# Kernel tuning notes

Measured on AMD Instinct MI355X. Metric: run time of the kernel, lower is better.

## Reference

```python
import jax, jax.numpy as jnp
import numpy as np

HEADS = 8
DH = 64          # value head dim == kernel head dim (expansion ratio 1.0)
DIM = 256
BOT = 256        # bottleneck_dim
DOUT = 256
HID = 4 * 256    # MLP hidden (expansion_ratio=4)
EPS_LN = 1e-5
EPS_GN = 1e-6


def layer_norm(x, g, b):
    m = x.mean(axis=-1, keepdims=True)
    v = x.var(axis=-1, keepdims=True)
    return (x - m) / jnp.sqrt(v + EPS_LN) * g + b


def rotate_half(x):
    x1, x2 = jnp.split(x, 2, axis=-1)
    return jnp.concatenate([-x2, x1], axis=-1)


def apply_rope(t, cos, sin):
    return t * cos + rotate_half(t) * sin


def mlp(x, W1, b1, W2, b2):
    return jax.nn.gelu(x @ W1 + b1) @ W2 + b2


def pooling_reducer(x, Win, W1, b1, W2, b2):
    # x: (b, n, m, c); mean-pool over axis 2, then MLP
    x = x @ Win
    x = x.mean(axis=2)
    return mlp(x, W1, b1, W2, b2)


def dp_kernel(x, Wqk, cos, sin):
    # x: (b, n, BOT) -> softmax attention kernel (b, h, n, n)
    b, n, _ = x.shape
    qk = (x @ Wqk).reshape(b, n, 2, HEADS, DH).transpose(0, 3, 2, 1, 4)  # b h 2 n d
    qk = apply_rope(qk, cos, sin)
    q, k = qk[:, :, 0], qk[:, :, 1]
    attn = jnp.einsum('bhid,bhjd->bhij', q, k) * (1.0 / DH)  # softmax scale = 1/dim_head
    return jax.nn.softmax(attn, axis=-1)


def group_norm(x):
    # channels-last GroupNorm(heads groups, affine=False), per position
    b, i, l, _ = x.shape
    xg = x.reshape(b, i, l, HEADS, DH)
    m = xg.mean(axis=-1, keepdims=True)
    v = xg.var(axis=-1, keepdims=True)
    return ((xg - m) / jnp.sqrt(v + EPS_GN)).reshape(b, i, l, HEADS * DH)


def setup_inputs() -> dict:
    key = jax.random.key(0)
    ks = jax.random.split(key, 32)
    B, NY, NX = 4, 128, 128
    s = 0.02
    d = {
        'u': jax.random.normal(ks[0], (B, NY, NX, DIM), jnp.float32),
        'rotary_cos_y': jax.random.uniform(ks[1], (NY, DH), jnp.float32),
        'rotary_sin_y': jax.random.uniform(ks[2], (NY, DH), jnp.float32),
        'rotary_cos_x': jax.random.uniform(ks[3], (NX, DH), jnp.float32),
        'rotary_sin_x': jax.random.uniform(ks[4], (NX, DH), jnp.float32),
        'scalar_cond': jax.random.normal(ks[5], (B,), jnp.float32),
        # norms
        'ln1_g': jnp.ones((DIM,), jnp.float32), 'ln1_b': jnp.zeros((DIM,), jnp.float32),
        'ln2_g': jnp.ones((DIM,), jnp.float32), 'ln2_b': jnp.zeros((DIM,), jnp.float32),
        # to_v
        'Wv': jax.random.normal(ks[6], (DIM, HEADS * DH), jnp.float32) * s,
        # to_y PoolingReducer
        'Wy_in': jax.random.normal(ks[7], (DIM, DIM), jnp.float32) * s,
        'Wy1': jax.random.normal(ks[8], (DIM, HID), jnp.float32) * s,
        'by1': jnp.zeros((HID,), jnp.float32),
        'Wy2': jax.random.normal(ks[9], (HID, BOT), jnp.float32) * s,
        'by2': jnp.zeros((BOT,), jnp.float32),
        # to_x PoolingReducer
        'Wx_in': jax.random.normal(ks[10], (DIM, DIM), jnp.float32) * s,
        'Wx1': jax.random.normal(ks[11], (DIM, HID), jnp.float32) * s,
        'bx1': jnp.zeros((HID,), jnp.float32),
        'Wx2': jax.random.normal(ks[12], (HID, BOT), jnp.float32) * s,
        'bx2': jnp.zeros((BOT,), jnp.float32),
        # kernels
        'Wqk_x': jax.random.normal(ks[13], (BOT, 2 * HEADS * DH), jnp.float32) * s,
        'Wqk_y': jax.random.normal(ks[14], (BOT, 2 * HEADS * DH), jnp.float32) * s,
        # merge head
        'Wm': jax.random.normal(ks[15], (HEADS * DH, DOUT), jnp.float32) * s,
        'bm': jnp.zeros((DOUT,), jnp.float32),
        # ffn
        'Wf1': jax.random.normal(ks[16], (DOUT, 4 * DOUT), jnp.float32) * s,
        'bf1': jnp.zeros((4 * DOUT,), jnp.float32),
        'Wf2': jax.random.normal(ks[17], (4 * DOUT, DOUT), jnp.float32) * s,
        'bf2': jnp.zeros((DOUT,), jnp.float32),
    }
    return d


def reference(u, rotary_cos_y, rotary_sin_y, rotary_cos_x, rotary_sin_x, scalar_cond,
              ln1_g, ln1_b, ln2_g, ln2_b, Wv,
              Wy_in, Wy1, by1, Wy2, by2,
              Wx_in, Wx1, bx1, Wx2, bx2,
              Wqk_x, Wqk_y, Wm, bm, Wf1, bf1, Wf2, bf2):
    b, ny, nx, _ = u.shape
    u_skip = u
    un = layer_norm(u, ln1_g, ln1_b)
    # to_x: transpose grid then pool over (now) second spatial axis -> (b, nx, BOT)
    u_x = pooling_reducer(un.transpose(0, 2, 1, 3), Wx_in, Wx1, bx1, Wx2, bx2)
    # to_y: pool over nx -> (b, ny, BOT)
    u_y = pooling_reducer(un, Wy_in, Wy1, by1, Wy2, by2)
    k_x = dp_kernel(u_x, Wqk_x, rotary_cos_x, rotary_sin_x)  # (b,h,nx,nx)
    k_y = dp_kernel(u_y, Wqk_y, rotary_cos_y, rotary_sin_y)  # (b,h,ny,ny)
    # values: b i l (h c) -> b h i l c
    v = (un @ Wv).reshape(b, ny, nx, HEADS, DH).transpose(0, 3, 1, 2, 4)
    u_phi = jnp.einsum('bhij,bhjmc->bhimc', k_y, v)
    u_phi = jnp.einsum('bhlm,bhimc->bhilc', k_x, u_phi)
    u_phi = u_phi.transpose(0, 2, 3, 1, 4).reshape(b, ny, nx, HEADS * DH)
    u2 = group_norm(u_phi) @ Wm + bm + u_skip  # dropout is identity in eval
    out = mlp(layer_norm(u2, ln2_g, ln2_b), Wf1, bf1, Wf2, bf2) + u2
    return out
```

## Files before the change

### kernel.cpp

```cpp
#include <hip/hip_runtime.h>
#include <hip/hip_bf16.h>
#include <math.h>

#define NB 4
#define NY 128
#define NX 128
#define DIM 256
#define NH 8
#define DH_ 64
#define HDIM 512
#define HID 1024
#define NPOS (NB*NY*NX)

typedef __hip_bfloat16 bf16_t;
typedef __attribute__((ext_vector_type(8))) short short8;
typedef __attribute__((ext_vector_type(4))) float f32x4;

__device__ __forceinline__ float b2f(bf16_t x){ return __bfloat162float(x); }
__device__ __forceinline__ bf16_t f2b(float x){ return __float2bfloat16(x); }
__device__ __forceinline__ short f2s(float x){ bf16_t h = __float2bfloat16(x); return *reinterpret_cast<short*>(&h); }
__device__ __forceinline__ float s2f(short x){ bf16_t h = *reinterpret_cast<bf16_t*>(&x); return __bfloat162float(h); }


__device__ __forceinline__ float gelu_tanh(float x){
  float z = 1.5957691216057308f*(x + 0.044715f*x*x*x);
  return x / (1.0f + __expf(-z));
}

__global__ void __launch_bounds__(256) k_pack(const float* __restrict__ W,
    short* __restrict__ out, int K, int N){
  int tid = blockIdx.x*256 + threadIdx.x;
  int lane = tid & 63;
  int rem = tid >> 6;
  int ntiles = N >> 4;
  int nt = rem % ntiles, kb = rem / ntiles;
  int n = nt*16 + (lane & 15);
  int k0 = kb*32 + (lane>>4)*8;
  short8 v;
  #pragma unroll
  for (int j=0;j<8;j++) v[j] = f2s(W[(size_t)(k0+j)*N + n]);
  *(short8*)&out[(size_t)tid*8] = v;
}

__global__ void __launch_bounds__(256) k_ln1(const float* __restrict__ u,
    const float* __restrict__ g, const float* __restrict__ b,
    bf16_t* __restrict__ un){
  int wave = threadIdx.x >> 6, lane = threadIdx.x & 63;
  size_t row = (size_t)blockIdx.x*4 + wave;
  const float* x = u + row*DIM;
  float v[4]; float s=0.f, ss=0.f;
  #pragma unroll
  for (int j=0;j<4;j++){ float t = x[lane + j*64]; v[j]=t; s+=t; ss+=t*t; }
  #pragma unroll
  for (int off=32;off>0;off>>=1){ s += __shfl_down(s,off,64); ss += __shfl_down(ss,off,64); }
  s = __shfl(s,0,64); ss = __shfl(ss,0,64);
  float m = s*(1.0f/DIM);
  float var = ss*(1.0f/DIM) - m*m;
  float r = rsqrtf(var + 1e-5f);
  bf16_t* o = un + row*DIM;
  #pragma unroll
  for (int j=0;j<4;j++){
    int f = lane + j*64;
    o[f] = f2b((v[j]-m)*r*g[f] + b[f]);
  }
}

__global__ void __launch_bounds__(256) k_pool_y(const bf16_t* __restrict__ un, float* __restrict__ pooly){
  int by = blockIdx.x;
  int d = threadIdx.x;
  size_t base = (size_t)by*NX*DIM + d;
  float s = 0.f;
  for (int x=0;x<NX;x++) s += b2f(un[base + (size_t)x*DIM]);
  pooly[(size_t)by*DIM + d] = s*(1.0f/NX);
}
__global__ void __launch_bounds__(256) k_pool_x(const bf16_t* __restrict__ un, float* __restrict__ poolx){
  int bb = blockIdx.x / NX, x = blockIdx.x % NX;
  int d = threadIdx.x;
  size_t base = ((size_t)bb*NY*NX + x)*DIM + d;
  float s = 0.f;
  for (int y=0;y<NY;y++) s += b2f(un[base + (size_t)y*NX*DIM]);
  poolx[(size_t)blockIdx.x*DIM + d] = s*(1.0f/NY);
}

#define GS_STRIDE 72
__global__ void __launch_bounds__(256) k_gemm2(const float* __restrict__ A0,
    const float* __restrict__ A1,
    const short* __restrict__ W0, const short* __restrict__ W1,
    const float* __restrict__ b0, const float* __restrict__ b1,
    float* __restrict__ C0, float* __restrict__ C1, int N, int K, int dogelu){
  const float* A  = blockIdx.z ? A1 : A0;
  const short* WP = blockIdx.z ? W1 : W0;
  const float* bias = blockIdx.z ? b1 : b0;
  float* C = blockIdx.z ? C1 : C0;
  __shared__ __align__(16) short As[64*GS_STRIDE];
  int tid = threadIdx.x;
  int lane = tid & 63, w = tid >> 6;
  int am = lane & 15, aq = lane >> 4;
  int m0 = blockIdx.x*64;
  int nt0 = blockIdx.y*16;
  int ntiles = N >> 4;
  f32x4 o[4][4];
  #pragma unroll
  for (int mt=0;mt<4;mt++)
    #pragma unroll
    for (int nt=0;nt<4;nt++) o[mt][nt] = (f32x4){0.f,0.f,0.f,0.f};

  for (int kc=0; kc<K; kc+=64){
    #pragma unroll
    for (int it=0; it<4; it++){
      int q = tid + it*256;
      int r = q >> 4, c4 = q & 15;
      float4 v = *(const float4*)&A[(size_t)(m0+r)*K + kc + c4*4];
      ushort4 p;
      p.x = (ushort)f2s(v.x); p.y = (ushort)f2s(v.y);
      p.z = (ushort)f2s(v.z); p.w = (ushort)f2s(v.w);
      *(ushort4*)&As[r*GS_STRIDE + c4*4] = p;
    }
    __syncthreads();
    #pragma unroll
    for (int kb=0; kb<2; kb++){
      short8 a[4], bfr[4];
      #pragma unroll
      for (int mt=0;mt<4;mt++)
        a[mt] = *(const short8*)&As[(mt*16+am)*GS_STRIDE + kb*32 + aq*8];
      int kbg = (kc>>5) + kb;
      #pragma unroll
      for (int nt=0;nt<4;nt++){
        int ntg = nt0 + w*4 + nt;
        bfr[nt] = *(const short8*)&WP[(size_t)((kbg*ntiles + ntg)*64 + lane)*8];
      }
      #pragma unroll
      for (int mt=0;mt<4;mt++)
        #pragma unroll
        for (int nt=0;nt<4;nt++)
          o[mt][nt] = __builtin_amdgcn_mfma_f32_16x16x32_bf16(a[mt], bfr[nt], o[mt][nt], 0,0,0);
    }
    __syncthreads();
  }

  #pragma unroll
  for (int nt=0;nt<4;nt++){
    int col = (nt0 + w*4 + nt)*16 + am;
    float bv = bias ? bias[col] : 0.f;
    #pragma unroll
    for (int mt=0;mt<4;mt++){
      #pragma unroll
      for (int reg=0;reg<4;reg++){
        int row = m0 + mt*16 + aq*4 + reg;
        float val = o[mt][nt][reg] + bv;
        if (dogelu) val = gelu_tanh(val);
        C[(size_t)row*N + col] = val;
      }
    }
  }
}

__global__ void __launch_bounds__(256) k_rope(const float* __restrict__ qk,
    const float* __restrict__ cs, const float* __restrict__ sn,
    float* __restrict__ q, float* __restrict__ k){
  int idx = blockIdx.x*256 + threadIdx.x;
  int c = idx & 63;
  int h = (idx>>6) & 7;
  int p = (idx>>9) & 1;
  int n = (idx>>10) & 127;
  int bb = idx>>17;
  float t = qk[idx];
  float t2 = qk[(c<32) ? idx+32 : idx-32];
  if (c<32) t2 = -t2;
  float val = t*cs[n*64+c] + t2*sn[n*64+c];
  float* dst = p ? k : q;
  dst[(((size_t)bb*NH + h)*128 + n)*64 + c] = val;
}

__global__ void __launch_bounds__(128) k_attn(const float* __restrict__ q,
    const float* __restrict__ k, bf16_t* __restrict__ attn){
  int i = blockIdx.x & 127;
  int bh = blockIdx.x >> 7;
  __shared__ float qs[64];
  __shared__ float red[4];
  int tid = threadIdx.x;
  int wv = tid >> 6, lane = tid & 63;
  const float* qrow = q + ((size_t)bh*128 + i)*64;
  if (tid < 64) qs[tid] = qrow[tid];
  __syncthreads();
  const float* krow = k + ((size_t)bh*128 + tid)*64;
  float dot = 0.f;
  for (int c=0;c<64;c++) dot += qs[c]*krow[c];
  dot *= (1.0f/64.0f);
  float mx = dot;
  #pragma unroll
  for (int off=32;off>0;off>>=1) mx = fmaxf(mx, __shfl_xor(mx, off, 64));
  if (lane == 0) red[wv] = mx;
  __syncthreads();
  mx = fmaxf(red[0], red[1]);
  float e = __expf(dot - mx);
  float s = e;
  #pragma unroll
  for (int off=32;off>0;off>>=1) s += __shfl_xor(s, off, 64);
  if (lane == 0) red[2+wv] = s;
  __syncthreads();
  s = red[2] + red[3];
  attn[(size_t)blockIdx.x*128 + tid] = f2b(e/s);
}

#define AST 136
#define UST 72
#define VST 136
__global__ void __launch_bounds__(512) k_phi1m(const bf16_t* __restrict__ un,
    const short* __restrict__ WvP, const bf16_t* __restrict__ attn,
    bf16_t* __restrict__ phi){
  int m  = blockIdx.x & (NX-1);
  int bh = blockIdx.x >> 7;
  int b  = bh >> 3, h = bh & 7;
  __shared__ __align__(16) short At[128*AST];
  __shared__ __align__(16) short unc[128*UST];
  __shared__ __align__(16) short Vt[64*VST];
  int tid = threadIdx.x;
  int lane = tid & 63, w = tid >> 6;
  int am = lane & 15, aq = lane >> 4;

  {
    const ushort* ag = (const ushort*)attn + (size_t)bh*16384;
    #pragma unroll
    for (int it=0; it<8; it++){
      int q = tid + it*512;
      int i = q >> 5, j4 = q & 31;
      *(ushort4*)&At[i*AST + j4*4] = *(const ushort4*)(ag + i*128 + j4*4);
    }
  }

  f32x4 v[4];
  #pragma unroll
  for (int nt=0;nt<4;nt++) v[nt] = (f32x4){0.f,0.f,0.f,0.f};
  const ushort* ug = (const ushort*)un;
  for (int kc=0; kc<4; kc++){
    #pragma unroll
    for (int it=0; it<4; it++){
      int q = tid + it*512;
      int y = q >> 4, c4 = q & 15;
      *(ushort4*)&unc[y*UST + c4*4] =
          *(const ushort4*)(ug + (((size_t)b*NY + y)*NX + m)*DIM + kc*64 + c4*4);
    }
    __syncthreads();
    #pragma unroll
    for (int kb=0; kb<2; kb++){
      short8 a2 = *(const short8*)&unc[(w*16 + am)*UST + kb*32 + aq*8];
      int kbg = kc*2 + kb;
      short8 bb[4];
      #pragma unroll
      for (int nt=0;nt<4;nt++)
        bb[nt] = *(const short8*)&WvP[(size_t)((kbg*32 + (h*4+nt))*64 + lane)*8];
      #pragma unroll
      for (int nt=0;nt<4;nt++)
        v[nt] = __builtin_amdgcn_mfma_f32_16x16x32_bf16(a2, bb[nt], v[nt], 0,0,0);
    }
    __syncthreads();
  }
  #pragma unroll
  for (int nt=0;nt<4;nt++){
    int c = nt*16 + am;
    int y0 = w*16 + aq*4;
    ushort4 pk;
    pk.x = (ushort)f2s(v[nt][0]);
    pk.y = (ushort)f2s(v[nt][1]);
    pk.z = (ushort)f2s(v[nt][2]);
    pk.w = (ushort)f2s(v[nt][3]);
    *(ushort4*)&Vt[c*VST + y0] = pk;
  }
  __syncthreads();

  f32x4 o[4];
  #pragma unroll
  for (int nt=0;nt<4;nt++) o[nt] = (f32x4){0.f,0.f,0.f,0.f};
  #pragma unroll
  for (int kb=0; kb<4; kb++){
    short8 a2 = *(const short8*)&At[(w*16 + am)*AST + kb*32 + aq*8];
    short8 bb[4];
    #pragma unroll
    for (int nt=0;nt<4;nt++)
      bb[nt] = *(const short8*)&Vt[(nt*16 + am)*VST + kb*32 + aq*8];
    #pragma unroll
    for (int nt=0;nt<4;nt++)
      o[nt] = __builtin_amdgcn_mfma_f32_16x16x32_bf16(a2, bb[nt], o[nt], 0,0,0);
  }
  ushort* pg = (ushort*)phi + (size_t)bh*NY*NX*DH_ + (size_t)m*DH_;
  #pragma unroll
  for (int nt=0;nt<4;nt++)
    #pragma unroll
    for (int reg=0;reg<4;reg++){
      int i = w*16 + aq*4 + reg;
      int c = nt*16 + am;
      pg[(size_t)i*(NX*DH_) + c] = (ushort)f2s(o[nt][reg]);
    }
}

__global__ void __launch_bounds__(512) k_phi2m(const bf16_t* __restrict__ attn,
    bf16_t* __restrict__ phi){
  int i  = blockIdx.x & (NY-1);
  int bh = blockIdx.x >> 7;
  __shared__ __align__(16) short Ax[128*AST];
  __shared__ __align__(16) short Pt[64*VST];
  int tid = threadIdx.x;
  int lane = tid & 63, w = tid >> 6;
  int am = lane & 15, aq = lane >> 4;

  {
    const ushort* ag = (const ushort*)attn + (size_t)bh*16384;
    #pragma unroll
    for (int it=0; it<8; it++){
      int q = tid + it*512;
      int r = q >> 5, j4 = q & 31;
      *(ushort4*)&Ax[r*AST + j4*4] = *(const ushort4*)(ag + r*128 + j4*4);
    }
  }
  ushort* pg = (ushort*)phi + (size_t)(bh*NY + i)*(NX*DH_);
  #pragma unroll
  for (int it=0; it<4; it++){
    int q = tid + it*512;
    int mm = q >> 4, c4 = q & 15;
    ushort4 v4 = *(const ushort4*)(pg + mm*DH_ + c4*4);
    Pt[(c4*4+0)*VST + mm] = v4.x;
    Pt[(c4*4+1)*VST + mm] = v4.y;
    Pt[(c4*4+2)*VST + mm] = v4.z;
    Pt[(c4*4+3)*VST + mm] = v4.w;
  }
  __syncthreads();

  f32x4 o[4];
  #pragma unroll
  for (int nt=0;nt<4;nt++) o[nt] = (f32x4){0.f,0.f,0.f,0.f};
  #pragma unroll
  for (int kb=0; kb<4; kb++){
    short8 a2 = *(const short8*)&Ax[(w*16 + am)*AST + kb*32 + aq*8];
    short8 bb[4];
    #pragma unroll
    for (int nt=0;nt<4;nt++)
      bb[nt] = *(const short8*)&Pt[(nt*16 + am)*VST + kb*32 + aq*8];
    #pragma unroll
    for (int nt=0;nt<4;nt++)
      o[nt] = __builtin_amdgcn_mfma_f32_16x16x32_bf16(a2, bb[nt], o[nt], 0,0,0);
  }
  #pragma unroll
  for (int reg=0;reg<4;reg++){
    float s  = o[0][reg]+o[1][reg]+o[2][reg]+o[3][reg];
    float ss = o[0][reg]*o[0][reg]+o[1][reg]*o[1][reg]
             + o[2][reg]*o[2][reg]+o[3][reg]*o[3][reg];
    #pragma unroll
    for (int msk=1; msk<16; msk<<=1){
      s  += __shfl_xor(s,  msk, 64);
      ss += __shfl_xor(ss, msk, 64);
    }
    float mm = s*(1.0f/64.0f);
    float vv = ss*(1.0f/64.0f) - mm*mm;
    float rs = rsqrtf(vv + 1e-6f);
    #pragma unroll
    for (int nt=0;nt<4;nt++)
      o[nt][reg] = (o[nt][reg]-mm)*rs;
  }
  #pragma unroll
  for (int nt=0;nt<4;nt++)
    #pragma unroll
    for (int reg=0;reg<4;reg++){
      int l = w*16 + aq*4 + reg;
      int c = nt*16 + am;
      pg[(size_t)l*DH_ + c] = (ushort)f2s(o[nt][reg]);
    }
}

#define GN_ST 520
#define ML_ST 264
__global__ void __launch_bounds__(512, 4) k_tail(const bf16_t* __restrict__ phi,
    const short* __restrict__ WmP, const float* __restrict__ bm,
    const float* __restrict__ u,
    const float* __restrict__ g2, const float* __restrict__ b2,
    const short* __restrict__ Wf1P, const float* __restrict__ bf1,
    const short* __restrict__ Wf2P, const float* __restrict__ bf2,
    float* __restrict__ out){
  __shared__ __align__(16) short SMEM[64*ML_ST*2];
  __shared__ float prow[64][4], prow2[64][4];
  __shared__ float mrow[64], rrow[64];
  short* Xg = SMEM;
  short* Xm = SMEM;
  short* H  = SMEM + 64*ML_ST;
  int tid = threadIdx.x;
  int lane = tid & 63, w = tid >> 6;
  int wh = w >> 2, wl = w & 3;
  int am = lane & 15, aq = lane >> 4;
  size_t p0 = (size_t)blockIdx.x*64;
  int b  = (int)(p0 >> 14);
  int y  = (int)((p0 >> 7) & 127);
  int x0 = (int)(p0 & 127);

  #pragma unroll
  for (int it=0; it<16; it++){
    int q = tid + it*512;
    int r = q >> 7, f4 = q & 127;
    int h = f4 >> 4, c4 = f4 & 15;
    size_t gi = (((size_t)b*NH + h)*NY + y)*NX + (x0 + r);
    *(ushort4*)&Xg[r*GN_ST + f4*4] =
        *(const ushort4*)((const ushort*)phi + gi*DH_ + c4*4);
  }
  __syncthreads();

  f32x4 u2r[2][4];
  #pragma unroll
  for (int mt=0;mt<2;mt++)
    #pragma unroll
    for (int nt=0;nt<4;nt++) u2r[mt][nt] = (f32x4){0.f,0.f,0.f,0.f};
  for (int kb=0; kb<16; kb++){
    short8 a[2], bfr[4];
    #pragma unroll
    for (int mt=0;mt<2;mt++)
      a[mt] = *(const short8*)&Xg[(wh*32 + mt*16 + am)*GN_ST + kb*32 + aq*8];
    #pragma unroll
    for (int nt=0;nt<4;nt++)
      bfr[nt] = *(const short8*)&WmP[(size_t)((kb*16 + (wl*4+nt))*64 + lane)*8];
    #pragma unroll
    for (int mt=0;mt<2;mt++)
      #pragma unroll
      for (int nt=0;nt<4;nt++)
        u2r[mt][nt] = __builtin_amdgcn_mfma_f32_16x16x32_bf16(a[mt], bfr[nt], u2r[mt][nt], 0,0,0);
  }
  #pragma unroll
  for (int nt=0;nt<4;nt++){
    int col = wl*64 + nt*16 + am;
    float bmv = bm[col];
    #pragma unroll
    for (int mt=0;mt<2;mt++){
      #pragma unroll
      for (int reg=0;reg<4;reg++){
        size_t p = p0 + wh*32 + mt*16 + aq*4 + reg;
        u2r[mt][nt][reg] += bmv + u[p*DIM + col];
      }
    }
  }

  #pragma unroll
  for (int mt=0;mt<2;mt++){
    #pragma unroll
    for (int reg=0;reg<4;reg++){
      float s  = u2r[mt][0][reg]+u2r[mt][1][reg]+u2r[mt][2][reg]+u2r[mt][3][reg];
      float ss = u2r[mt][0][reg]*u2r[mt][0][reg]+u2r[mt][1][reg]*u2r[mt][1][reg]
               + u2r[mt][2][reg]*u2r[mt][2][reg]+u2r[mt][3][reg]*u2r[mt][3][reg];
      #pragma unroll
      for (int msk=1; msk<16; msk<<=1){
        s  += __shfl_xor(s,  msk, 64);
        ss += __shfl_xor(ss, msk, 64);
      }
      if (am == 0){
        int r = wh*32 + mt*16 + aq*4 + reg;
        prow[r][wl] = s;
        prow2[r][wl] = ss;
      }
    }
  }
  __syncthreads();
  if (tid < 64){
    float s  = prow[tid][0]+prow[tid][1]+prow[tid][2]+prow[tid][3];
    float ss = prow2[tid][0]+prow2[tid][1]+prow2[tid][2]+prow2[tid][3];
    float m = s*(1.0f/DIM);
    mrow[tid] = m;
    rrow[tid] = rsqrtf(ss*(1.0f/DIM) - m*m + 1e-5f);
  }
  __syncthreads();
  #pragma unroll
  for (int nt=0;nt<4;nt++){
    int col = wl*64 + nt*16 + am;
    float gg = g2[col], bb2 = b2[col];
    #pragma unroll
    for (int mt=0;mt<2;mt++){
      #pragma unroll
      for (int reg=0;reg<4;reg++){
        int r = wh*32 + mt*16 + aq*4 + reg;
        Xm[r*ML_ST + col] = f2s((u2r[mt][nt][reg]-mrow[r])*rrow[r]*gg + bb2);
      }
    }
  }
  __syncthreads();

  f32x4 o2[2][4];
  #pragma unroll
  for (int mt=0;mt<2;mt++)
    #pragma unroll
    for (int nt=0;nt<4;nt++) o2[mt][nt] = u2r[mt][nt];

  for (int nc=0; nc<4; nc++){
    f32x4 hacc[2][4];
    #pragma unroll
    for (int mt=0;mt<2;mt++)
      #pragma unroll
      for (int nt=0;nt<4;nt++) hacc[mt][nt] = (f32x4){0.f,0.f,0.f,0.f};
    for (int kb=0; kb<8; kb++){
      short8 a[2], bfr[4];
      #pragma unroll
      for (int mt=0;mt<2;mt++)
        a[mt] = *(const short8*)&Xm[(wh*32 + mt*16 + am)*ML_ST + kb*32 + aq*8];
      #pragma unroll
      for (int nt=0;nt<4;nt++){
        int ntg = nc*16 + wl*4 + nt;
        bfr[nt] = *(const short8*)&Wf1P[(size_t)((kb*64 + ntg)*64 + lane)*8];
      }
      #pragma unroll
      for (int mt=0;mt<2;mt++)
        #pragma unroll
        for (int nt=0;nt<4;nt++)
          hacc[mt][nt] = __builtin_amdgcn_mfma_f32_16x16x32_bf16(a[mt], bfr[nt], hacc[mt][nt], 0,0,0);
    }
    #pragma unroll
    for (int nt=0;nt<4;nt++){
      int col_l = wl*64 + nt*16 + am;
      float bv = bf1[nc*256 + col_l];
      #pragma unroll
      for (int mt=0;mt<2;mt++){
        #pragma unroll
        for (int reg=0;reg<4;reg++){
          int row = wh*32 + mt*16 + aq*4 + reg;
          H[row*ML_ST + col_l] = f2s(gelu_tanh(hacc[mt][nt][reg] + bv));
        }
      }
    }
    __syncthreads();
    for (int kb=0; kb<8; kb++){
      short8 a[2], bfr[4];
      #pragma unroll
      for (int mt=0;mt<2;mt++)
        a[mt] = *(const short8*)&H[(wh*32 + mt*16 + am)*ML_ST + kb*32 + aq*8];
      int kbg = nc*8 + kb;
      #pragma unroll
      for (int nt=0;nt<4;nt++)
        bfr[nt] = *(const short8*)&Wf2P[(size_t)((kbg*16 + (wl*4+nt))*64 + lane)*8];
      #pragma unroll
      for (int mt=0;mt<2;mt++)
        #pragma unroll
        for (int nt=0;nt<4;nt++)
          o2[mt][nt] = __builtin_amdgcn_mfma_f32_16x16x32_bf16(a[mt], bfr[nt], o2[mt][nt], 0,0,0);
    }
    __syncthreads();
  }

  #pragma unroll
  for (int nt=0;nt<4;nt++){
    int col = wl*64 + nt*16 + am;
    float bv = bf2[col];
    #pragma unroll
    for (int mt=0;mt<2;mt++){
      #pragma unroll
      for (int reg=0;reg<4;reg++){
        size_t p = p0 + wh*32 + mt*16 + aq*4 + reg;
        out[p*DIM + col] = o2[mt][nt][reg] + bv;
      }
    }
  }
}

extern "C" void kernel_launch(void* const* d_in, const int* in_sizes, int n_in,
                              void* d_out, int out_size, void* d_ws, size_t ws_size,
                              hipStream_t stream){
  const float* u    = (const float*)d_in[0];
  const float* rcy  = (const float*)d_in[1];
  const float* rsy  = (const float*)d_in[2];
  const float* rcx  = (const float*)d_in[3];
  const float* rsx  = (const float*)d_in[4];
  const float* ln1g = (const float*)d_in[6];
  const float* ln1b = (const float*)d_in[7];
  const float* ln2g = (const float*)d_in[8];
  const float* ln2b = (const float*)d_in[9];
  const float* Wv   = (const float*)d_in[10];
  const float* Wyin = (const float*)d_in[11];
  const float* Wy1  = (const float*)d_in[12];
  const float* by1  = (const float*)d_in[13];
  const float* Wy2  = (const float*)d_in[14];
  const float* by2  = (const float*)d_in[15];
  const float* Wxin = (const float*)d_in[16];
  const float* Wx1  = (const float*)d_in[17];
  const float* bx1  = (const float*)d_in[18];
  const float* Wx2  = (const float*)d_in[19];
  const float* bx2  = (const float*)d_in[20];
  const float* Wqkx = (const float*)d_in[21];
  const float* Wqky = (const float*)d_in[22];
  const float* Wm   = (const float*)d_in[23];
  const float* bm   = (const float*)d_in[24];
  const float* Wf1  = (const float*)d_in[25];
  const float* bf1  = (const float*)d_in[26];
  const float* Wf2  = (const float*)d_in[27];
  const float* bf2  = (const float*)d_in[28];

  char* w = (char*)d_ws;
  auto alloc = [&](size_t n) -> void* {
    void* p = (void*)w;
    w += (n + 255) & ~(size_t)255;
    return p;
  };
  bf16_t* UN   = (bf16_t*)alloc((size_t)NPOS*DIM*2);
  bf16_t* PHI  = (bf16_t*)alloc((size_t)NB*NH*NY*NX*DH_*2);
  float* POOLY = (float*)alloc((size_t)NB*NY*DIM*4);
  float* POOLX = (float*)alloc((size_t)NB*NX*DIM*4);
  float* TY    = (float*)alloc((size_t)512*256*4);
  float* TX    = (float*)alloc((size_t)512*256*4);
  float* HY    = (float*)alloc((size_t)512*1024*4);
  float* HX    = (float*)alloc((size_t)512*1024*4);
  float* UY    = (float*)alloc((size_t)512*256*4);
  float* UX    = (float*)alloc((size_t)512*256*4);
  float* QKY   = (float*)alloc((size_t)512*1024*4);
  float* QKX   = (float*)alloc((size_t)512*1024*4);
  float* QRY   = (float*)alloc((size_t)NB*NH*128*64*4);
  float* KRY   = (float*)alloc((size_t)NB*NH*128*64*4);
  float* QRX   = (float*)alloc((size_t)NB*NH*128*64*4);
  float* KRX   = (float*)alloc((size_t)NB*NH*128*64*4);
  bf16_t* ATTNY = (bf16_t*)alloc((size_t)NB*NH*128*128*2);
  bf16_t* ATTNX = (bf16_t*)alloc((size_t)NB*NH*128*128*2);
  short* WF1P  = (short*)alloc((size_t)256*1024*2);
  short* WF2P  = (short*)alloc((size_t)1024*256*2);
  short* WMP   = (short*)alloc((size_t)512*256*2);
  short* WVP   = (short*)alloc((size_t)256*512*2);
  short* WYINP = (short*)alloc((size_t)256*256*2);
  short* WY1P  = (short*)alloc((size_t)256*1024*2);
  short* WY2P  = (short*)alloc((size_t)1024*256*2);
  short* WQKYP = (short*)alloc((size_t)256*1024*2);
  short* WXINP = (short*)alloc((size_t)256*256*2);
  short* WX1P  = (short*)alloc((size_t)256*1024*2);
  short* WX2P  = (short*)alloc((size_t)1024*256*2);
  short* WQKXP = (short*)alloc((size_t)256*1024*2);
  float* U2 = (float*)d_out;
  (void)in_sizes; (void)n_in; (void)out_size; (void)ws_size;

  k_pack<<<(256*1024/8)/256, 256, 0, stream>>>(Wf1, WF1P, 256, 1024);
  k_pack<<<(1024*256/8)/256, 256, 0, stream>>>(Wf2, WF2P, 1024, 256);
  k_pack<<<(512*256/8)/256, 256, 0, stream>>>(Wm, WMP, 512, 256);
  k_pack<<<(256*512/8)/256, 256, 0, stream>>>(Wv, WVP, 256, 512);
  k_pack<<<(256*256/8)/256, 256, 0, stream>>>(Wyin, WYINP, 256, 256);
  k_pack<<<(256*1024/8)/256, 256, 0, stream>>>(Wy1, WY1P, 256, 1024);
  k_pack<<<(1024*256/8)/256, 256, 0, stream>>>(Wy2, WY2P, 1024, 256);
  k_pack<<<(256*1024/8)/256, 256, 0, stream>>>(Wqky, WQKYP, 256, 1024);
  k_pack<<<(256*256/8)/256, 256, 0, stream>>>(Wxin, WXINP, 256, 256);
  k_pack<<<(256*1024/8)/256, 256, 0, stream>>>(Wx1, WX1P, 256, 1024);
  k_pack<<<(1024*256/8)/256, 256, 0, stream>>>(Wx2, WX2P, 1024, 256);
  k_pack<<<(256*1024/8)/256, 256, 0, stream>>>(Wqkx, WQKXP, 256, 1024);

  k_ln1<<<NPOS/4, 256, 0, stream>>>(u, ln1g, ln1b, UN);
  k_pool_y<<<NB*NY, 256, 0, stream>>>(UN, POOLY);
  k_pool_x<<<NB*NX, 256, 0, stream>>>(UN, POOLX);

  k_gemm2<<<dim3(8,1,2), 256, 0, stream>>>(POOLY, POOLX, WYINP, WXINP,
      (const float*)nullptr, (const float*)nullptr, TY, TX, 256, 256, 0);
  k_gemm2<<<dim3(8,4,2), 256, 0, stream>>>(TY, TX, WY1P, WX1P, by1, bx1, HY, HX, 1024, 256, 1);
  k_gemm2<<<dim3(8,1,2), 256, 0, stream>>>(HY, HX, WY2P, WX2P, by2, bx2, UY, UX, 256, 1024, 0);
  k_gemm2<<<dim3(8,4,2), 256, 0, stream>>>(UY, UX, WQKYP, WQKXP,
      (const float*)nullptr, (const float*)nullptr, QKY, QKX, 1024, 256, 0);

  k_rope<<<(NB*128*1024)/256, 256, 0, stream>>>(QKY, rcy, rsy, QRY, KRY);
  k_rope<<<(NB*128*1024)/256, 256, 0, stream>>>(QKX, rcx, rsx, QRX, KRX);
  k_attn<<<NB*NH*128, 128, 0, stream>>>(QRY, KRY, ATTNY);
  k_attn<<<NB*NH*128, 128, 0, stream>>>(QRX, KRX, ATTNX);
  k_phi1m<<<NB*NH*NX, 512, 0, stream>>>(UN, WVP, ATTNY, PHI);
  k_phi2m<<<NB*NH*NY, 512, 0, stream>>>(ATTNX, PHI);
  k_tail<<<NPOS/64, 512, 0, stream>>>(PHI, WMP, bm, u, ln2g, ln2b,
      WF1P, bf1, WF2P, bf2, U2);
}
```

Baseline: 620.4 us.

## Batch weight packing and rope/attn launches, split pooling, prefetch tail weights

Replaces twelve weight-pack launches with one batched kernel, merges the y/x rope and attention launches into single 2D-grid launches, and splits each pooling reduction over four thread groups with a shared-memory combine. In the tail kernel, the residual and bias are loaded into the accumulators before the GEMM, and the packed weight fragments for the next k-step are register-prefetched in all three GEMM loops. The aims are less launch overhead, more parallelism in pooling, and hiding global weight-load latency behind MFMAs, at the cost of more registers in the tail kernel.

```diff
diff --git a/kernel.cpp b/kernel.cpp
--- a/kernel.cpp
+++ b/kernel.cpp
@@ -27,9 +27,21 @@
   return x / (1.0f + __expf(-z));
 }
 
-__global__ void __launch_bounds__(256) k_pack(const float* __restrict__ W,
-    short* __restrict__ out, int K, int N){
-  int tid = blockIdx.x*256 + threadIdx.x;
+struct PackArgs {
+  const float* src[12];
+  short* dst[12];
+  int K[12];
+  int N[12];
+  int boff[12];
+};
+__global__ void __launch_bounds__(256) k_pack_all(PackArgs pa){
+  int idx = 0;
+  #pragma unroll
+  for (int j=1;j<12;j++) if ((int)blockIdx.x >= pa.boff[j]) idx = j;
+  int tid = ((int)blockIdx.x - pa.boff[idx])*256 + threadIdx.x;
+  const float* W = pa.src[idx];
+  short* out = pa.dst[idx];
+  int N = pa.N[idx];
   int lane = tid & 63;
   int rem = tid >> 6;
   int ntiles = N >> 4;
@@ -65,21 +77,31 @@
   }
 }
 
-__global__ void __launch_bounds__(256) k_pool_y(const bf16_t* __restrict__ un, float* __restrict__ pooly){
+__global__ void __launch_bounds__(1024) k_pool_y(const bf16_t* __restrict__ un, float* __restrict__ pooly){
   int by = blockIdx.x;
-  int d = threadIdx.x;
+  int d = threadIdx.x & 255, xq = threadIdx.x >> 8;
+  __shared__ float part[4][256];
   size_t base = (size_t)by*NX*DIM + d;
   float s = 0.f;
-  for (int x=0;x<NX;x++) s += b2f(un[base + (size_t)x*DIM]);
-  pooly[(size_t)by*DIM + d] = s*(1.0f/NX);
-}
-__global__ void __launch_bounds__(256) k_pool_x(const bf16_t* __restrict__ un, float* __restrict__ poolx){
+  int x0 = xq*32;
+  for (int x=x0; x<x0+32; x++) s += b2f(un[base + (size_t)x*DIM]);
+  part[xq][d] = s;
+  __syncthreads();
+  if (threadIdx.x < 256)
+    pooly[(size_t)by*DIM + d] = (part[0][d]+part[1][d]+part[2][d]+part[3][d])*(1.0f/NX);
+}
+__global__ void __launch_bounds__(1024) k_pool_x(const bf16_t* __restrict__ un, float* __restrict__ poolx){
   int bb = blockIdx.x / NX, x = blockIdx.x % NX;
-  int d = threadIdx.x;
+  int d = threadIdx.x & 255, yq = threadIdx.x >> 8;
+  __shared__ float part[4][256];
   size_t base = ((size_t)bb*NY*NX + x)*DIM + d;
   float s = 0.f;
-  for (int y=0;y<NY;y++) s += b2f(un[base + (size_t)y*NX*DIM]);
-  poolx[(size_t)blockIdx.x*DIM + d] = s*(1.0f/NY);
+  int y0 = yq*32;
+  for (int y=y0; y<y0+32; y++) s += b2f(un[base + (size_t)y*NX*DIM]);
+  part[yq][d] = s;
+  __syncthreads();
+  if (threadIdx.x < 256)
+    poolx[(size_t)blockIdx.x*DIM + d] = (part[0][d]+part[1][d]+part[2][d]+part[3][d])*(1.0f/NY);
 }
 
 #define GS_STRIDE 72
@@ -155,9 +177,17 @@
   }
 }
 
-__global__ void __launch_bounds__(256) k_rope(const float* __restrict__ qk,
-    const float* __restrict__ cs, const float* __restrict__ sn,
-    float* __restrict__ q, float* __restrict__ k){
+__global__ void __launch_bounds__(256) k_rope2(const float* __restrict__ qky,
+    const float* __restrict__ qkx,
+    const float* __restrict__ csy, const float* __restrict__ sny,
+    const float* __restrict__ csx, const float* __restrict__ snx,
+    float* __restrict__ qy, float* __restrict__ ky,
+    float* __restrict__ qx, float* __restrict__ kx){
+  const float* qk = blockIdx.y ? qkx : qky;
+  const float* cs = blockIdx.y ? csx : csy;
+  const float* sn = blockIdx.y ? snx : sny;
+  float* q = blockIdx.y ? qx : qy;
+  float* k = blockIdx.y ? kx : ky;
   int idx = blockIdx.x*256 + threadIdx.x;
   int c = idx & 63;
   int h = (idx>>6) & 7;
@@ -172,8 +202,13 @@
   dst[(((size_t)bb*NH + h)*128 + n)*64 + c] = val;
 }
 
-__global__ void __launch_bounds__(128) k_attn(const float* __restrict__ q,
-    const float* __restrict__ k, bf16_t* __restrict__ attn){
+__global__ void __launch_bounds__(128) k_attn2(const float* __restrict__ qy,
+    const float* __restrict__ ky, bf16_t* __restrict__ ay,
+    const float* __restrict__ qx, const float* __restrict__ kx,
+    bf16_t* __restrict__ ax){
+  const float* q = blockIdx.y ? qx : qy;
+  const float* k = blockIdx.y ? kx : ky;
+  bf16_t* attn = blockIdx.y ? ax : ay;
   int i = blockIdx.x & 127;
   int bh = blockIdx.x >> 7;
   __shared__ float qs[64];
@@ -400,27 +435,7 @@
     *(ushort4*)&Xg[r*GN_ST + f4*4] =
         *(const ushort4*)((const ushort*)phi + gi*DH_ + c4*4);
   }
-  __syncthreads();
-
   f32x4 u2r[2][4];
-  #pragma unroll
-  for (int mt=0;mt<2;mt++)
-    #pragma unroll
-    for (int nt=0;nt<4;nt++) u2r[mt][nt] = (f32x4){0.f,0.f,0.f,0.f};
-  for (int kb=0; kb<16; kb++){
-    short8 a[2], bfr[4];
-    #pragma unroll
-    for (int mt=0;mt<2;mt++)
-      a[mt] = *(const short8*)&Xg[(wh*32 + mt*16 + am)*GN_ST + kb*32 + aq*8];
-    #pragma unroll
-    for (int nt=0;nt<4;nt++)
-      bfr[nt] = *(const short8*)&WmP[(size_t)((kb*16 + (wl*4+nt))*64 + lane)*8];
-    #pragma unroll
-    for (int mt=0;mt<2;mt++)
-      #pragma unroll
-      for (int nt=0;nt<4;nt++)
-        u2r[mt][nt] = __builtin_amdgcn_mfma_f32_16x16x32_bf16(a[mt], bfr[nt], u2r[mt][nt], 0,0,0);
-  }
   #pragma unroll
   for (int nt=0;nt<4;nt++){
     int col = wl*64 + nt*16 + am;
@@ -430,8 +445,36 @@
       #pragma unroll
       for (int reg=0;reg<4;reg++){
         size_t p = p0 + wh*32 + mt*16 + aq*4 + reg;
-        u2r[mt][nt][reg] += bmv + u[p*DIM + col];
-      }
+        u2r[mt][nt][reg] = bmv + u[p*DIM + col];
+      }
+    }
+  }
+  __syncthreads();
+
+  {
+    short8 wnext[4];
+    #pragma unroll
+    for (int nt=0;nt<4;nt++)
+      wnext[nt] = *(const short8*)&WmP[(size_t)(((wl*4+nt))*64 + lane)*8];
+    #pragma unroll
+    for (int kb=0; kb<16; kb++){
+      short8 cw[4];
+      #pragma unroll
+      for (int nt=0;nt<4;nt++) cw[nt] = wnext[nt];
+      if (kb < 15){
+        #pragma unroll
+        for (int nt=0;nt<4;nt++)
+          wnext[nt] = *(const short8*)&WmP[(size_t)(((kb+1)*16 + (wl*4+nt))*64 + lane)*8];
+      }
+      short8 a[2];
+      #pragma unroll
+      for (int mt=0;mt<2;mt++)
+        a[mt] = *(const short8*)&Xg[(wh*32 + mt*16 + am)*GN_ST + kb*32 + aq*8];
+      #pragma unroll
+      for (int mt=0;mt<2;mt++)
+        #pragma unroll
+        for (int nt=0;nt<4;nt++)
+          u2r[mt][nt] = __builtin_amdgcn_mfma_f32_16x16x32_bf16(a[mt], cw[nt], u2r[mt][nt], 0,0,0);
     }
   }
 
@@ -490,21 +533,35 @@
     for (int mt=0;mt<2;mt++)
       #pragma unroll
       for (int nt=0;nt<4;nt++) hacc[mt][nt] = (f32x4){0.f,0.f,0.f,0.f};
-    for (int kb=0; kb<8; kb++){
-      short8 a[2], bfr[4];
-      #pragma unroll
-      for (int mt=0;mt<2;mt++)
-        a[mt] = *(const short8*)&Xm[(wh*32 + mt*16 + am)*ML_ST + kb*32 + aq*8];
+    {
+      short8 wnext[4];
       #pragma unroll
       for (int nt=0;nt<4;nt++){
         int ntg = nc*16 + wl*4 + nt;
-        bfr[nt] = *(const short8*)&Wf1P[(size_t)((kb*64 + ntg)*64 + lane)*8];
-      }
-      #pragma unroll
-      for (int mt=0;mt<2;mt++)
-        #pragma unroll
-        for (int nt=0;nt<4;nt++)
-          hacc[mt][nt] = __builtin_amdgcn_mfma_f32_16x16x32_bf16(a[mt], bfr[nt], hacc[mt][nt], 0,0,0);
+        wnext[nt] = *(const short8*)&Wf1P[(size_t)((ntg)*64 + lane)*8];
+      }
+      #pragma unroll
+      for (int kb=0; kb<8; kb++){
+        short8 cw[4];
+        #pragma unroll
+        for (int nt=0;nt<4;nt++) cw[nt] = wnext[nt];
+        if (kb < 7){
+          #pragma unroll
+          for (int nt=0;nt<4;nt++){
+            int ntg = nc*16 + wl*4 + nt;
+            wnext[nt] = *(const short8*)&Wf1P[(size_t)(((kb+1)*64 + ntg)*64 + lane)*8];
+          }
+        }
+        short8 a[2];
+        #pragma unroll
+        for (int mt=0;mt<2;mt++)
+          a[mt] = *(const short8*)&Xm[(wh*32 + mt*16 + am)*ML_ST + kb*32 + aq*8];
+        #pragma unroll
+        for (int mt=0;mt<2;mt++)
+          #pragma unroll
+          for (int nt=0;nt<4;nt++)
+            hacc[mt][nt] = __builtin_amdgcn_mfma_f32_16x16x32_bf16(a[mt], cw[nt], hacc[mt][nt], 0,0,0);
+      }
     }
     #pragma unroll
     for (int nt=0;nt<4;nt++){
@@ -520,20 +577,32 @@
       }
     }
     __syncthreads();
-    for (int kb=0; kb<8; kb++){
-      short8 a[2], bfr[4];
-      #pragma unroll
-      for (int mt=0;mt<2;mt++)
-        a[mt] = *(const short8*)&H[(wh*32 + mt*16 + am)*ML_ST + kb*32 + aq*8];
-      int kbg = nc*8 + kb;
+    {
+      short8 wnext[4];
       #pragma unroll
       for (int nt=0;nt<4;nt++)
-        bfr[nt] = *(const short8*)&Wf2P[(size_t)((kbg*16 + (wl*4+nt))*64 + lane)*8];
-      #pragma unroll
-      for (int mt=0;mt<2;mt++)
-        #pragma unroll
-        for (int nt=0;nt<4;nt++)
-          o2[mt][nt] = __builtin_amdgcn_mfma_f32_16x16x32_bf16(a[mt], bfr[nt], o2[mt][nt], 0,0,0);
+        wnext[nt] = *(const short8*)&Wf2P[(size_t)(((nc*8)*16 + (wl*4+nt))*64 + lane)*8];
+      #pragma unroll
+      for (int kb=0; kb<8; kb++){
+        short8 cw[4];
+        #pragma unroll
+        for (int nt=0;nt<4;nt++) cw[nt] = wnext[nt];
+        if (kb < 7){
+          int kbg = nc*8 + kb + 1;
+          #pragma unroll
+          for (int nt=0;nt<4;nt++)
+            wnext[nt] = *(const short8*)&Wf2P[(size_t)((kbg*16 + (wl*4+nt))*64 + lane)*8];
+        }
+        short8 a[2];
+        #pragma unroll
+        for (int mt=0;mt<2;mt++)
+          a[mt] = *(const short8*)&H[(wh*32 + mt*16 + am)*ML_ST + kb*32 + aq*8];
+        #pragma unroll
+        for (int mt=0;mt<2;mt++)
+          #pragma unroll
+          for (int nt=0;nt<4;nt++)
+            o2[mt][nt] = __builtin_amdgcn_mfma_f32_16x16x32_bf16(a[mt], cw[nt], o2[mt][nt], 0,0,0);
+      }
     }
     __syncthreads();
   }
@@ -624,22 +693,20 @@
   float* U2 = (float*)d_out;
   (void)in_sizes; (void)n_in; (void)out_size; (void)ws_size;
 
-  k_pack<<<(256*1024/8)/256, 256, 0, stream>>>(Wf1, WF1P, 256, 1024);
-  k_pack<<<(1024*256/8)/256, 256, 0, stream>>>(Wf2, WF2P, 1024, 256);
-  k_pack<<<(512*256/8)/256, 256, 0, stream>>>(Wm, WMP, 512, 256);
-  k_pack<<<(256*512/8)/256, 256, 0, stream>>>(Wv, WVP, 256, 512);
-  k_pack<<<(256*256/8)/256, 256, 0, stream>>>(Wyin, WYINP, 256, 256);
-  k_pack<<<(256*1024/8)/256, 256, 0, stream>>>(Wy1, WY1P, 256, 1024);
-  k_pack<<<(1024*256/8)/256, 256, 0, stream>>>(Wy2, WY2P, 1024, 256);
-  k_pack<<<(256*1024/8)/256, 256, 0, stream>>>(Wqky, WQKYP, 256, 1024);
-  k_pack<<<(256*256/8)/256, 256, 0, stream>>>(Wxin, WXINP, 256, 256);
-  k_pack<<<(256*1024/8)/256, 256, 0, stream>>>(Wx1, WX1P, 256, 1024);
-  k_pack<<<(1024*256/8)/256, 256, 0, stream>>>(Wx2, WX2P, 1024, 256);
-  k_pack<<<(256*1024/8)/256, 256, 0, stream>>>(Wqkx, WQKXP, 256, 1024);
+  PackArgs pa;
+  const float* srcs[12] = {Wf1,Wf2,Wm,Wv,Wyin,Wy1,Wy2,Wqky,Wxin,Wx1,Wx2,Wqkx};
+  short* dsts[12] = {WF1P,WF2P,WMP,WVP,WYINP,WY1P,WY2P,WQKYP,WXINP,WX1P,WX2P,WQKXP};
+  int Ks[12] = {256,1024,512,256,256,256,1024,256,256,256,1024,256};
+  int Ns[12] = {1024,256,256,512,256,1024,256,1024,256,1024,256,1024};
+  int boffs[12] = {0,128,256,320,384,416,544,672,800,832,960,1088};
+  for (int i=0;i<12;i++){
+    pa.src[i]=srcs[i]; pa.dst[i]=dsts[i]; pa.K[i]=Ks[i]; pa.N[i]=Ns[i]; pa.boff[i]=boffs[i];
+  }
+  k_pack_all<<<1216, 256, 0, stream>>>(pa);
 
   k_ln1<<<NPOS/4, 256, 0, stream>>>(u, ln1g, ln1b, UN);
-  k_pool_y<<<NB*NY, 256, 0, stream>>>(UN, POOLY);
-  k_pool_x<<<NB*NX, 256, 0, stream>>>(UN, POOLX);
+  k_pool_y<<<NB*NY, 1024, 0, stream>>>(UN, POOLY);
+  k_pool_x<<<NB*NX, 1024, 0, stream>>>(UN, POOLX);
 
   k_gemm2<<<dim3(8,1,2), 256, 0, stream>>>(POOLY, POOLX, WYINP, WXINP,
       (const float*)nullptr, (const float*)nullptr, TY, TX, 256, 256, 0);
@@ -648,10 +715,9 @@
   k_gemm2<<<dim3(8,4,2), 256, 0, stream>>>(UY, UX, WQKYP, WQKXP,
       (const float*)nullptr, (const float*)nullptr, QKY, QKX, 1024, 256, 0);
 
-  k_rope<<<(NB*128*1024)/256, 256, 0, stream>>>(QKY, rcy, rsy, QRY, KRY);
-  k_rope<<<(NB*128*1024)/256, 256, 0, stream>>>(QKX, rcx, rsx, QRX, KRX);
-  k_attn<<<NB*NH*128, 128, 0, stream>>>(QRY, KRY, ATTNY);
-  k_attn<<<NB*NH*128, 128, 0, stream>>>(QRX, KRX, ATTNX);
+  k_rope2<<<dim3((NB*128*1024)/256, 2), 256, 0, stream>>>(QKY, QKX,
+      rcy, rsy, rcx, rsx, QRY, KRY, QRX, KRX);
+  k_attn2<<<dim3(NB*NH*128, 2), 128, 0, stream>>>(QRY, KRY, ATTNY, QRX, KRX, ATTNX);
   k_phi1m<<<NB*NH*NX, 512, 0, stream>>>(UN, WVP, ATTNY, PHI);
   k_phi2m<<<NB*NH*NY, 512, 0, stream>>>(ATTNX, PHI);
   k_tail<<<NPOS/64, 512, 0, stream>>>(PHI, WMP, bm, u, ln2g, ln2b,
```

Result: slower. 643.5 us (+3.7%).
